# Performance work log

Hardware: AMD Instinct MI355X
Metric: run time of the kernel (lower is better)

The kernel has to match this reference:

```python
import jax, jax.numpy as jnp
import numpy as np

T, B, I, H = 1024, 64, 512, 512


def setup_inputs() -> dict:
    key = jax.random.key(0)
    ks = jax.random.split(key, 7)
    s = 1.0 / np.sqrt(H).astype(np.float32)
    return {
        "x": jax.random.normal(ks[0], (T, B, I), dtype=jnp.float32),
        "h0": jax.random.normal(ks[1], (B, H), dtype=jnp.float32),
        "c0": jax.random.normal(ks[2], (B, H), dtype=jnp.float32),
        "W_ih": jax.random.normal(ks[3], (4 * H, I), dtype=jnp.float32) * s,
        "W_hh": jax.random.normal(ks[4], (4 * H, H), dtype=jnp.float32) * s,
        "b_ih": jax.random.normal(ks[5], (4 * H,), dtype=jnp.float32) * s,
        "b_hh": jax.random.normal(ks[6], (4 * H,), dtype=jnp.float32) * s,
        "alpha": jnp.ones((1,), dtype=jnp.float32),
    }


def reference(x, h0, c0, W_ih, W_hh, b_ih, b_hh, alpha):
    # Precompute input-to-hidden projections for all timesteps in one GEMM.
    # x: [T, B, I] -> xg: [T, B, 4H]
    xg = jnp.einsum("tbi,gi->tbg", x, W_ih) + b_ih
    a = alpha[0]

    def step(carry, xg_t):
        h, c = carry  # [B, H] each
        gates = xg_t + h @ W_hh.T + b_hh  # [B, 4H]
        i, f, g, o = jnp.split(gates, 4, axis=-1)
        i = jax.nn.sigmoid(i)
        f = jax.nn.sigmoid(f)
        g = jnp.tanh(g)
        o = jax.nn.sigmoid(o)
        c_new = f * c + i * g
        h_new = o * jnp.tanh(c_new)
        # alpha step-size interpolation (alpha=1 -> plain LSTM)
        c_out = a * c_new + (1.0 - a) * c
        h_out = a * h_new + (1.0 - a) * h
        return (h_out, c_out), h_out

    (hT, cT), ys = jax.lax.scan(step, (h0, c0), xg)
    return ys, hT, cT
```

## Files before the change

kernel.cpp:

```cpp
#include <hip/hip_runtime.h>

typedef __attribute__((ext_vector_type(8))) short short8;
typedef __attribute__((ext_vector_type(4))) float f32x4;
typedef __attribute__((ext_vector_type(4))) float float4v;
typedef __attribute__((ext_vector_type(4))) unsigned short u16x4;
typedef __attribute__((ext_vector_type(4))) unsigned int u32x4;

#define T_TOT   1024
#define BATCH   64
#define HID     512
#define G4      2048
#define NGRID   128
#define BH      (BATCH * HID)

static __device__ __forceinline__ unsigned short f2bf(float x) {
  union { float f; unsigned u; } v; v.f = x;
  unsigned r = v.u + 0x7FFFu + ((v.u >> 16) & 1u);
  return (unsigned short)(r >> 16);
}
static __device__ __forceinline__ float sigm(float x) {
  return 1.0f / (1.0f + __expf(-x));
}
static __device__ __forceinline__ float tanh_fast(float x) {
  return 1.0f - 2.0f / (__expf(2.0f * x) + 1.0f);
}
static __device__ __forceinline__ void bar_lds() {
  asm volatile("s_waitcnt lgkmcnt(0)" ::: "memory");
  __builtin_amdgcn_s_barrier();
  asm volatile("" ::: "memory");
}

__global__ void init_k(const float* __restrict__ h0, const float* __restrict__ c0,
                       unsigned int* __restrict__ hb2, float* __restrict__ cst,
                       float* __restrict__ hst, unsigned int* __restrict__ fin) {
  const int i = blockIdx.x * 256 + threadIdx.x;
  if (i < T_TOT * NGRID) fin[i] = 0u;
  if (i < BH) {
    const float h = h0[i];
    hb2[i] = (unsigned)f2bf(h);
    hb2[BH + i] = 0xFFFF0000u;
    hst[i] = h;
    cst[i] = c0[i];
  }
}

__global__ __launch_bounds__(256) void xz_gemm(
    const float* __restrict__ A, const float* __restrict__ W,
    const float* __restrict__ bih, const float* __restrict__ bhh,
    float* __restrict__ xzp) {
  __shared__ unsigned short As[128 * 64];
  __shared__ unsigned short Bs[128 * 64];
  const int tid  = threadIdx.x;
  const int lane = tid & 63;
  const int wid  = tid >> 6;
  const int wm   = (wid >> 1) * 64;
  const int wn   = (wid & 1) * 64;
  const int l15  = lane & 15;
  const int l4   = lane >> 4;
  const long bm  = blockIdx.x;
  const long bn  = blockIdx.y;

  f32x4 acc[4][4];
#pragma unroll
  for (int mt = 0; mt < 4; ++mt)
#pragma unroll
    for (int nt = 0; nt < 4; ++nt) acc[mt][nt] = f32x4{0.f, 0.f, 0.f, 0.f};

  const float* Ab = A + bm * 128 * 512;
  const float* Wb = W + bn * 128 * 512;
  const int r0 = tid >> 4;
  const int cq = (tid & 15) * 4;

  for (int k0 = 0; k0 < 512; k0 += 64) {
#pragma unroll
    for (int pass = 0; pass < 8; ++pass) {
      const int r = pass * 16 + r0;
      const float4v va = *(const float4v*)(Ab + (long)r * 512 + k0 + cq);
      const float4v vb = *(const float4v*)(Wb + (long)r * 512 + k0 + cq);
      u16x4 pa, pb;
#pragma unroll
      for (int j = 0; j < 4; ++j) { pa[j] = f2bf(va[j]); pb[j] = f2bf(vb[j]); }
      const int boff = r * 128 + ((cq * 2) ^ ((r & 7) << 4));
      *(u16x4*)((char*)As + boff) = pa;
      *(u16x4*)((char*)Bs + boff) = pb;
    }
    __syncthreads();
#pragma unroll
    for (int kk = 0; kk < 2; ++kk) {
      short8 af[4], bfv[4];
#pragma unroll
      for (int mt = 0; mt < 4; ++mt) {
        const int row = wm + mt * 16 + l15;
        af[mt] = *(const short8*)((const char*)As + row * 128 +
                                  ((kk * 64 + l4 * 16) ^ ((row & 7) << 4)));
      }
#pragma unroll
      for (int nt = 0; nt < 4; ++nt) {
        const int row = wn + nt * 16 + l15;
        bfv[nt] = *(const short8*)((const char*)Bs + row * 128 +
                                   ((kk * 64 + l4 * 16) ^ ((row & 7) << 4)));
      }
#pragma unroll
      for (int mt = 0; mt < 4; ++mt)
#pragma unroll
        for (int nt = 0; nt < 4; ++nt)
          acc[mt][nt] = __builtin_amdgcn_mfma_f32_16x16x32_bf16(af[mt], bfv[nt], acc[mt][nt], 0, 0, 0);
    }
    __syncthreads();
  }

#pragma unroll
  for (int nt = 0; nt < 4; ++nt) {
    const int gn = (int)(bn * 128) + wn + nt * 16 + l15;
    const float bias = bih[gn] + bhh[gn];
    const int g2  = gn >> 9;
    const int hh  = gn & 511;
    const int nb2 = hh >> 4;
    const int en2 = hh & 15;
#pragma unroll
    for (int mt = 0; mt < 4; ++mt) {
      const int m0 = (int)(bm * 128) + wm + mt * 16 + l4 * 4;
#pragma unroll
      for (int r = 0; r < 4; ++r) {
        const int m = m0 + r;
        const int tt2 = m >> 6, brow = m & 63;
        const int mb2 = brow >> 4, em2 = brow & 15;
        xzp[((((size_t)tt2 * 4 + mb2) * 32 + nb2) << 10) + em2 * 64 + g2 * 16 + en2] =
            acc[mt][nt][r] + bias;
      }
    }
  }
}

__global__ __launch_bounds__(256, 1) void lstm_steps(
    const float* __restrict__ xzp,
    const float* __restrict__ Whh,
    const float* __restrict__ alpha_p,
    float* __restrict__ out,
    unsigned int* __restrict__ hb2,
    float* __restrict__ cst, float* __restrict__ hst,
    unsigned int* fin,
    int t0, int Tc) {
  const int bx  = blockIdx.x;
  const int mb  = bx >> 5;
  const int nb  = bx & 31;
  const int rb0 = mb * 16;
  const int hs0 = nb * 16;
  const int tid = threadIdx.x;
  const int lane = tid & 63;
  const int w   = tid >> 6;
  const int l15 = lane & 15;
  const int l4  = lane >> 4;

  __shared__ __align__(16) unsigned short h_lds[16 * HID];
  __shared__ __align__(16) float gates[4][16][20];

  short8 wf[16];
  {
    const float* wr = Whh + (long)(w * HID + hs0 + l15) * HID + l4 * 8;
#pragma unroll
    for (int ks = 0; ks < 16; ++ks) {
      const float4v lo = *(const float4v*)(wr + ks * 32);
      const float4v hi = *(const float4v*)(wr + ks * 32 + 4);
      short8 f;
#pragma unroll
      for (int j = 0; j < 4; ++j) {
        f[j]     = (short)f2bf(lo[j]);
        f[j + 4] = (short)f2bf(hi[j]);
      }
      wf[ks] = f;
    }
  }
  const float a = alpha_p[0];
  const float oma = 1.0f - a;

  const int em = tid >> 4;
  const int en = tid & 15;
  float cp = cst[(long)(rb0 + em) * HID + hs0 + en];
  float hp = hst[(long)(rb0 + em) * HID + hs0 + en];

  const long YS = (long)T_TOT * BATCH * HID;

  for (int tt = 0; tt < Tc; ++tt) {
    const int t = t0 + tt;

    f32x4 acc[4];
    {
      const float* xb = xzp + ((((size_t)tt * 4 + mb) * 32 + nb) << 10) +
                        w * 16 + l15;
#pragma unroll
      for (int r = 0; r < 4; ++r) acc[0][r] = xb[(l4 * 4 + r) * 64];
    }
    acc[1] = f32x4{0.f, 0.f, 0.f, 0.f};
    acc[2] = acc[1];
    acc[3] = acc[1];

    if (t > 0) {
      const unsigned int* fl = fin + ((size_t)(t - 1) * 4 + mb) * 32;
      while (true) {
        const unsigned v = __hip_atomic_load(&fl[lane & 31], __ATOMIC_RELAXED,
                                             __HIP_MEMORY_SCOPE_AGENT);
        if (__all(v != 0)) break;
      }
      asm volatile("" ::: "memory");
    }

    u32x4 sa[4], sb[4];
    {
      const unsigned int* p0 = hb2 + (size_t)(t & 1) * BH +
                               (size_t)(rb0 + w) * HID + lane * 8;
#pragma unroll
      for (int i = 0; i < 4; ++i) {
        const unsigned int* p = p0 + (size_t)i * 4 * HID;
        asm volatile("global_load_dwordx4 %0, %1, off sc0 sc1" : "=v"(sa[i]) : "v"(p));
        asm volatile("global_load_dwordx4 %0, %1, off sc0 sc1" : "=v"(sb[i]) : "v"(p + 4));
      }
      const unsigned wantHi = ((unsigned)t) << 16;
      for (;;) {
        asm volatile("s_waitcnt vmcnt(0)" ::: "memory");
        __builtin_amdgcn_sched_barrier(0);
        unsigned bad = 0u;
#pragma unroll
        for (int i = 0; i < 4; ++i) {
          unsigned d = 0u;
#pragma unroll
          for (int j = 0; j < 4; ++j)
            d |= ((sa[i][j] ^ wantHi) | (sb[i][j] ^ wantHi));
          if (d & 0xFFFF0000u) bad |= (1u << i);
        }
        if (!__any(bad)) break;
#pragma unroll
        for (int i = 0; i < 4; ++i)
          if (bad & (1u << i)) {
            const unsigned int* p = p0 + (size_t)i * 4 * HID;
            asm volatile("global_load_dwordx4 %0, %1, off sc0 sc1" : "=v"(sa[i]) : "v"(p));
            asm volatile("global_load_dwordx4 %0, %1, off sc0 sc1" : "=v"(sb[i]) : "v"(p + 4));
          }
      }
    }

#pragma unroll
    for (int i = 0; i < 4; ++i) {
      u32x4 pk;
      pk[0] = __builtin_amdgcn_perm(sa[i][1], sa[i][0], 0x05040100u);
      pk[1] = __builtin_amdgcn_perm(sa[i][3], sa[i][2], 0x05040100u);
      pk[2] = __builtin_amdgcn_perm(sb[i][1], sb[i][0], 0x05040100u);
      pk[3] = __builtin_amdgcn_perm(sb[i][3], sb[i][2], 0x05040100u);
      const int r = 4 * i + w;
      const int c = lane;
      *(u32x4*)((char*)h_lds + c * 256 + ((r ^ (c & 15)) << 4)) = pk;
    }
    bar_lds();

#pragma unroll
    for (int ks = 0; ks < 16; ++ks) {
      const int c = ks * 4 + l4;
      const short8 af = *(const short8*)((const char*)h_lds + c * 256 +
                                         ((l15 ^ (c & 15)) << 4));
      acc[ks & 3] = __builtin_amdgcn_mfma_f32_16x16x32_bf16(af, wf[ks], acc[ks & 3], 0, 0, 0);
    }
    {
      const f32x4 s = (acc[0] + acc[1]) + (acc[2] + acc[3]);
#pragma unroll
      for (int r = 0; r < 4; ++r)
        gates[w][l4 * 4 + r][l15] = s[r];
    }
    bar_lds();

    const float gi = gates[0][em][en], gf = gates[1][em][en];
    const float gg = gates[2][em][en], go = gates[3][em][en];
    const float ii = sigm(gi), ff = sigm(gf), oo = sigm(go);
    const float g  = tanh_fast(gg);
    const float cn = ff * cp + ii * g;
    const float hn = oo * tanh_fast(cn);
    const float co = a * cn + oma * cp;
    const float ho = a * hn + oma * hp;
    cp = co;
    hp = ho;

    {
      unsigned int* dst = hb2 + (size_t)((t + 1) & 1) * BH +
                          (long)(rb0 + em) * HID + hs0 + en;
      const unsigned w32 = (((unsigned)(t + 1)) << 16) | (unsigned)f2bf(ho);
      asm volatile("global_store_dword %0, %1, off sc0 sc1"
                   :: "v"((const void*)dst), "v"(w32) : "memory");
    }
    __builtin_amdgcn_s_barrier();
    asm volatile("" ::: "memory");
    if (tid == 0)
      __hip_atomic_store(&fin[((size_t)t * 4 + mb) * 32 + nb], 1u,
                         __ATOMIC_RELAXED, __HIP_MEMORY_SCOPE_AGENT);

    out[((long)t * BATCH + rb0 + em) * HID + hs0 + en] = ho;
    if (t == T_TOT - 1) {
      out[YS + (long)(rb0 + em) * HID + hs0 + en] = ho;
      out[YS + BATCH * HID + (long)(rb0 + em) * HID + hs0 + en] = co;
    }
  }

  cst[(long)(rb0 + em) * HID + hs0 + en] = cp;
  hst[(long)(rb0 + em) * HID + hs0 + en] = hp;
}

extern "C" void kernel_launch(void* const* d_in, const int* in_sizes, int n_in,
                              void* d_out, int out_size, void* d_ws, size_t ws_size,
                              hipStream_t stream) {
  const float* x     = (const float*)d_in[0];
  const float* h0    = (const float*)d_in[1];
  const float* c0    = (const float*)d_in[2];
  const float* W_ih  = (const float*)d_in[3];
  const float* W_hh  = (const float*)d_in[4];
  const float* b_ih  = (const float*)d_in[5];
  const float* b_hh  = (const float*)d_in[6];
  const float* alpha = (const float*)d_in[7];
  float* out = (float*)d_out;

  char* ws = (char*)d_ws;
  unsigned int* fin = (unsigned int*)(ws + 0);
  unsigned int* hb2 = (unsigned int*)(ws + 524288);
  float* cst = (float*)(ws + 786432);
  float* hst = (float*)(ws + 917504);
  float* xzp = (float*)(ws + 1048576);

  int Tc = T_TOT;
  while ((size_t)Tc * 524288ull + 1048576ull > ws_size && Tc > 2) Tc >>= 1;

  init_k<<<512, 256, 0, stream>>>(h0, c0, hb2, cst, hst, fin);
  for (int t0 = 0; t0 < T_TOT; t0 += Tc) {
    dim3 gg(Tc / 2, 16);
    xz_gemm<<<gg, 256, 0, stream>>>(x + (size_t)t0 * BATCH * 512,
                                    W_ih, b_ih, b_hh, xzp);
    lstm_steps<<<NGRID, 256, 0, stream>>>(xzp, W_hh, alpha, out, hb2,
                                          cst, hst, fin, t0, Tc);
  }
}
```

Before: 3.021 ms.

## Drop per-step flag barrier, rely on tagged h values and prefetch next step

Removes the separate per-timestep completion flag array and its spin-wait. Blocks now rely only on the step tag embedded in each packed bf16 h word to detect readiness. The next step's xz slice and h loads are issued right after the current step's h store, so their latency overlaps the wait for other blocks. The per-step output store is moved into the prefetch tail, with the last step's output written after the loop. This cuts one global synchronisation round trip per step, but correctness now depends on the tag check alone, and a prefetch that lands early simply triggers a retry.

```diff
diff --git a/kernel.cpp b/kernel.cpp
--- a/kernel.cpp
+++ b/kernel.cpp
@@ -32,9 +32,8 @@
 
 __global__ void init_k(const float* __restrict__ h0, const float* __restrict__ c0,
                        unsigned int* __restrict__ hb2, float* __restrict__ cst,
-                       float* __restrict__ hst, unsigned int* __restrict__ fin) {
+                       float* __restrict__ hst) {
   const int i = blockIdx.x * 256 + threadIdx.x;
-  if (i < T_TOT * NGRID) fin[i] = 0u;
   if (i < BH) {
     const float h = h0[i];
     hb2[i] = (unsigned)f2bf(h);
@@ -139,7 +138,6 @@
     float* __restrict__ out,
     unsigned int* __restrict__ hb2,
     float* __restrict__ cst, float* __restrict__ hst,
-    unsigned int* fin,
     int t0, int Tc) {
   const int bx  = blockIdx.x;
   const int mb  = bx >> 5;
@@ -181,44 +179,35 @@
 
   const long YS = (long)T_TOT * BATCH * HID;
 
+  float xz0, xz1, xz2, xz3;
+  u32x4 sa[4], sb[4];
+  {
+    const float* xb = xzp + (((size_t)0 * 4 + mb) * 32 + nb) * 1024 + w * 16 + l15;
+    asm volatile("global_load_dword %0, %1, off" : "=v"(xz0) : "v"(xb + (l4 * 4 + 0) * 64));
+    asm volatile("global_load_dword %0, %1, off" : "=v"(xz1) : "v"(xb + (l4 * 4 + 1) * 64));
+    asm volatile("global_load_dword %0, %1, off" : "=v"(xz2) : "v"(xb + (l4 * 4 + 2) * 64));
+    asm volatile("global_load_dword %0, %1, off" : "=v"(xz3) : "v"(xb + (l4 * 4 + 3) * 64));
+    const unsigned int* p0 = hb2 + (size_t)(t0 & 1) * BH + (size_t)(rb0 + w) * HID + lane * 8;
+#pragma unroll
+    for (int i = 0; i < 4; ++i) {
+      const unsigned int* p = p0 + (size_t)i * 4 * HID;
+      asm volatile("global_load_dwordx4 %0, %1, off sc0 sc1" : "=v"(sa[i]) : "v"(p));
+      asm volatile("global_load_dwordx4 %0, %1, off sc0 sc1" : "=v"(sb[i]) : "v"(p + 4));
+    }
+  }
+
   for (int tt = 0; tt < Tc; ++tt) {
     const int t = t0 + tt;
 
-    f32x4 acc[4];
+    if (tt == 0) asm volatile("s_waitcnt vmcnt(0)" ::: "memory");
+    else         asm volatile("s_waitcnt vmcnt(1)" ::: "memory");
+    __builtin_amdgcn_sched_barrier(0);
+
     {
-      const float* xb = xzp + ((((size_t)tt * 4 + mb) * 32 + nb) << 10) +
-                        w * 16 + l15;
-#pragma unroll
-      for (int r = 0; r < 4; ++r) acc[0][r] = xb[(l4 * 4 + r) * 64];
-    }
-    acc[1] = f32x4{0.f, 0.f, 0.f, 0.f};
-    acc[2] = acc[1];
-    acc[3] = acc[1];
-
-    if (t > 0) {
-      const unsigned int* fl = fin + ((size_t)(t - 1) * 4 + mb) * 32;
-      while (true) {
-        const unsigned v = __hip_atomic_load(&fl[lane & 31], __ATOMIC_RELAXED,
-                                             __HIP_MEMORY_SCOPE_AGENT);
-        if (__all(v != 0)) break;
-      }
-      asm volatile("" ::: "memory");
-    }
-
-    u32x4 sa[4], sb[4];
-    {
+      const unsigned wantHi = ((unsigned)t) << 16;
       const unsigned int* p0 = hb2 + (size_t)(t & 1) * BH +
                                (size_t)(rb0 + w) * HID + lane * 8;
-#pragma unroll
-      for (int i = 0; i < 4; ++i) {
-        const unsigned int* p = p0 + (size_t)i * 4 * HID;
-        asm volatile("global_load_dwordx4 %0, %1, off sc0 sc1" : "=v"(sa[i]) : "v"(p));
-        asm volatile("global_load_dwordx4 %0, %1, off sc0 sc1" : "=v"(sb[i]) : "v"(p + 4));
-      }
-      const unsigned wantHi = ((unsigned)t) << 16;
       for (;;) {
-        asm volatile("s_waitcnt vmcnt(0)" ::: "memory");
-        __builtin_amdgcn_sched_barrier(0);
         unsigned bad = 0u;
 #pragma unroll
         for (int i = 0; i < 4; ++i) {
@@ -228,7 +217,7 @@
             d |= ((sa[i][j] ^ wantHi) | (sb[i][j] ^ wantHi));
           if (d & 0xFFFF0000u) bad |= (1u << i);
         }
-        if (!__any(bad)) break;
+        if (!__any(bad != 0u)) break;
 #pragma unroll
         for (int i = 0; i < 4; ++i)
           if (bad & (1u << i)) {
@@ -236,6 +225,8 @@
             asm volatile("global_load_dwordx4 %0, %1, off sc0 sc1" : "=v"(sa[i]) : "v"(p));
             asm volatile("global_load_dwordx4 %0, %1, off sc0 sc1" : "=v"(sb[i]) : "v"(p + 4));
           }
+        asm volatile("s_waitcnt vmcnt(0)" ::: "memory");
+        __builtin_amdgcn_sched_barrier(0);
       }
     }
 
@@ -252,6 +243,11 @@
     }
     bar_lds();
 
+    f32x4 acc[4];
+    acc[0][0] = xz0; acc[0][1] = xz1; acc[0][2] = xz2; acc[0][3] = xz3;
+    acc[1] = f32x4{0.f, 0.f, 0.f, 0.f};
+    acc[2] = acc[1];
+    acc[3] = acc[1];
 #pragma unroll
     for (int ks = 0; ks < 16; ++ks) {
       const int c = ks * 4 + l4;
@@ -285,21 +281,38 @@
       asm volatile("global_store_dword %0, %1, off sc0 sc1"
                    :: "v"((const void*)dst), "v"(w32) : "memory");
     }
-    __builtin_amdgcn_s_barrier();
-    asm volatile("" ::: "memory");
-    if (tid == 0)
-      __hip_atomic_store(&fin[((size_t)t * 4 + mb) * 32 + nb], 1u,
-                         __ATOMIC_RELAXED, __HIP_MEMORY_SCOPE_AGENT);
-
-    out[((long)t * BATCH + rb0 + em) * HID + hs0 + en] = ho;
-    if (t == T_TOT - 1) {
-      out[YS + (long)(rb0 + em) * HID + hs0 + en] = ho;
-      out[YS + BATCH * HID + (long)(rb0 + em) * HID + hs0 + en] = co;
-    }
-  }
-
-  cst[(long)(rb0 + em) * HID + hs0 + en] = cp;
-  hst[(long)(rb0 + em) * HID + hs0 + en] = hp;
+
+    if (tt < Tc - 1) {
+      const float* xb = xzp + (((size_t)(tt + 1) * 4 + mb) * 32 + nb) * 1024 +
+                        w * 16 + l15;
+      asm volatile("global_load_dword %0, %1, off" : "=v"(xz0) : "v"(xb + (l4 * 4 + 0) * 64));
+      asm volatile("global_load_dword %0, %1, off" : "=v"(xz1) : "v"(xb + (l4 * 4 + 1) * 64));
+      asm volatile("global_load_dword %0, %1, off" : "=v"(xz2) : "v"(xb + (l4 * 4 + 2) * 64));
+      asm volatile("global_load_dword %0, %1, off" : "=v"(xz3) : "v"(xb + (l4 * 4 + 3) * 64));
+      const unsigned int* pn = hb2 + (size_t)((t + 1) & 1) * BH +
+                               (size_t)(rb0 + w) * HID + lane * 8;
+#pragma unroll
+      for (int i = 0; i < 4; ++i) {
+        const unsigned int* p = pn + (size_t)i * 4 * HID;
+        asm volatile("global_load_dwordx4 %0, %1, off sc0 sc1" : "=v"(sa[i]) : "v"(p));
+        asm volatile("global_load_dwordx4 %0, %1, off sc0 sc1" : "=v"(sb[i]) : "v"(p + 4));
+      }
+      const float* op = out + ((long)t * BATCH + rb0 + em) * HID + hs0 + en;
+      asm volatile("global_store_dword %0, %1, off"
+                   :: "v"((const void*)op), "v"(ho) : "memory");
+    }
+  }
+
+  {
+    const int tl = t0 + Tc - 1;
+    out[((long)tl * BATCH + rb0 + em) * HID + hs0 + en] = hp;
+    if (t0 + Tc == T_TOT) {
+      out[YS + (long)(rb0 + em) * HID + hs0 + en] = hp;
+      out[YS + BATCH * HID + (long)(rb0 + em) * HID + hs0 + en] = cp;
+    }
+    cst[(long)(rb0 + em) * HID + hs0 + en] = cp;
+    hst[(long)(rb0 + em) * HID + hs0 + en] = hp;
+  }
 }
 
 extern "C" void kernel_launch(void* const* d_in, const int* in_sizes, int n_in,
@@ -316,21 +329,20 @@
   float* out = (float*)d_out;
 
   char* ws = (char*)d_ws;
-  unsigned int* fin = (unsigned int*)(ws + 0);
-  unsigned int* hb2 = (unsigned int*)(ws + 524288);
-  float* cst = (float*)(ws + 786432);
-  float* hst = (float*)(ws + 917504);
-  float* xzp = (float*)(ws + 1048576);
+  unsigned int* hb2 = (unsigned int*)(ws + 0);
+  float* cst = (float*)(ws + 262144);
+  float* hst = (float*)(ws + 393216);
+  float* xzp = (float*)(ws + 524288);
 
   int Tc = T_TOT;
-  while ((size_t)Tc * 524288ull + 1048576ull > ws_size && Tc > 2) Tc >>= 1;
-
-  init_k<<<512, 256, 0, stream>>>(h0, c0, hb2, cst, hst, fin);
+  while ((size_t)Tc * 524288ull + 524288ull > ws_size && Tc > 2) Tc >>= 1;
+
+  init_k<<<128, 256, 0, stream>>>(h0, c0, hb2, cst, hst);
   for (int t0 = 0; t0 < T_TOT; t0 += Tc) {
     dim3 gg(Tc / 2, 16);
     xz_gemm<<<gg, 256, 0, stream>>>(x + (size_t)t0 * BATCH * 512,
                                     W_ih, b_ih, b_hh, xzp);
     lstm_steps<<<NGRID, 256, 0, stream>>>(xzp, W_hh, alpha, out, hb2,
-                                          cst, hst, fin, t0, Tc);
-  }
-}
+                                          cst, hst, t0, Tc);
+  }
+}
```

Measured after the change: 2.947 ms. -2.5%, faster.
